# Performance work log

Measured on AMD Instinct MI355X. Metric: run time of the kernel, lower is better.

Reference implementation:

```python
import jax, jax.numpy as jnp
import numpy as np

PAD = 0
VALUE_WEIGHT = 5.0
L, D, H, DF, V, T_MAX = 8, 1024, 16, 4096, 4096, 2048
HD = D // H


def _ln(x, w, b, eps=1e-5):
    mu = x.mean(-1, keepdims=True)
    var = ((x - mu) ** 2).mean(-1, keepdims=True)
    return (x - mu) * jax.lax.rsqrt(var + eps) * w + b


def setup_inputs() -> dict:
    key = jax.random.key(0)
    ks = jax.random.split(key, 16)
    s = 0.02
    inp = {
        'input_ids': jax.random.randint(ks[0], (4, 2048), 0, V),
        'targets': jax.random.randint(ks[1], (4, 2048), 0, V),
        'value_mask': jax.random.randint(ks[2], (4, 2048), 0, 2).astype(bool),
        'token_emb': jax.random.normal(ks[3], (V, D), jnp.float32) * s,
        'pos_emb': jax.random.normal(ks[4], (T_MAX, D), jnp.float32) * s,
        'ln1_w': jnp.ones((L, D), jnp.float32), 'ln1_b': jnp.zeros((L, D), jnp.float32),
        'wqkv': jax.random.normal(ks[5], (L, D, 3 * D), jnp.float32) * s,
        'bqkv': jnp.zeros((L, 3 * D), jnp.float32),
        'wproj': jax.random.normal(ks[6], (L, D, D), jnp.float32) * s,
        'bproj': jnp.zeros((L, D), jnp.float32),
        'ln2_w': jnp.ones((L, D), jnp.float32), 'ln2_b': jnp.zeros((L, D), jnp.float32),
        'w1': jax.random.normal(ks[7], (L, D, DF), jnp.float32) * s,
        'b1': jnp.zeros((L, DF), jnp.float32),
        'w2': jax.random.normal(ks[8], (L, DF, D), jnp.float32) * s,
        'b2': jnp.zeros((L, D), jnp.float32),
        'lnf_w': jnp.ones((D,), jnp.float32), 'lnf_b': jnp.zeros((D,), jnp.float32),
    }
    return inp


def reference(input_ids, targets, value_mask, token_emb, pos_emb, ln1_w, ln1_b,
              wqkv, bqkv, wproj, bproj, ln2_w, ln2_b, w1, b1, w2, b2, lnf_w, lnf_b):
    B, T = input_ids.shape
    x = token_emb[input_ids] + pos_emb[:T]  # (B,T,D)
    causal = jnp.triu(jnp.ones((T, T), bool), 1)  # True above diagonal -> masked
    scale = 1.0 / np.sqrt(HD)
    for l in range(L):
        h = _ln(x, ln1_w[l], ln1_b[l])
        qkv = h @ wqkv[l] + bqkv[l]  # (B,T,3D)
        q, k, v = jnp.split(qkv, 3, axis=-1)
        q = q.reshape(B, T, H, HD).transpose(0, 2, 1, 3)  # (B,H,T,HD)
        k = k.reshape(B, T, H, HD).transpose(0, 2, 1, 3)
        v = v.reshape(B, T, H, HD).transpose(0, 2, 1, 3)
        scores = jnp.einsum('bhqd,bhkd->bhqk', q, k) * scale
        scores = jnp.where(causal, -jnp.inf, scores)
        attn = jax.nn.softmax(scores, axis=-1)
        out = jnp.einsum('bhqk,bhkd->bhqd', attn, v)
        out = out.transpose(0, 2, 1, 3).reshape(B, T, D)
        x = x + out @ wproj[l] + bproj[l]
        h2 = _ln(x, ln2_w[l], ln2_b[l])
        x = x + jax.nn.gelu(h2 @ w1[l] + b1[l], approximate=False) @ w2[l] + b2[l]
    x = _ln(x, lnf_w, lnf_b)
    logits = x @ token_emb.T  # tied lm_head, (B,T,V)
    # weighted CE (ignore_index=PAD zeroes the per-token loss; weights sum over all tokens)
    logp = jax.nn.log_softmax(logits, axis=-1)
    nll = -jnp.take_along_axis(logp, targets[..., None], axis=-1)[..., 0]  # (B,T)
    ce = jnp.where(targets == PAD, 0.0, nll)
    weights = 1.0 + (VALUE_WEIGHT - 1.0) * value_mask.astype(jnp.float32)
    loss = (ce * weights).sum() / weights.sum()
    return logits, loss
```

## Files before the change

kernel.cpp:

```cpp
#include <hip/hip_runtime.h>
#include <hip/hip_bf16.h>

typedef unsigned short u16;
typedef short bf16x8 __attribute__((ext_vector_type(8)));
typedef float f32x4 __attribute__((ext_vector_type(4)));

__device__ inline float bflo(unsigned int w) { union { float f; unsigned int i; } c; c.i = w << 16; return c.f; }
__device__ inline float bfhi(unsigned int w) { union { float f; unsigned int i; } c; c.i = w & 0xffff0000u; return c.f; }
__device__ inline u16 f2bf(float f) {
    union { float f; unsigned int i; } c; c.f = f;
    unsigned int r = c.i + 0x7FFFu + ((c.i >> 16) & 1u);
    return (u16)(r >> 16);
}

__device__ inline float wave_sum(float v) {
#pragma unroll
    for (int off = 32; off; off >>= 1) v += __shfl_down(v, off);
    return v;
}

__device__ inline void gload16(const void* g, void* l) {
    __builtin_amdgcn_global_load_lds((const __attribute__((address_space(1))) void*)g,
                                     (__attribute__((address_space(3))) void*)l, 16, 0, 0);
}

__global__ __launch_bounds__(256) void k_cvt(const float* __restrict__ in, u16* __restrict__ out) {
    int i = blockIdx.x * 256 + threadIdx.x;
    float4 v = ((const float4*)in)[i];
    ushort4 o;
    o.x = f2bf(v.x); o.y = f2bf(v.y); o.z = f2bf(v.z); o.w = f2bf(v.w);
    ((ushort4*)out)[i] = o;
}

__global__ __launch_bounds__(256) void k_transpose(const float* __restrict__ in, u16* __restrict__ out, int R, int C) {
    __shared__ float tile[32][33];
    const float* inL = in + (size_t)blockIdx.z * R * C;
    u16* outL = out + (size_t)blockIdx.z * R * C;
    int cb = blockIdx.x * 32, rb = blockIdx.y * 32;
    int tx = threadIdx.x, ty = threadIdx.y;
#pragma unroll
    for (int i = 0; i < 32; i += 8)
        tile[ty + i][tx] = inL[(size_t)(rb + ty + i) * C + cb + tx];
    __syncthreads();
#pragma unroll
    for (int i = 0; i < 32; i += 8)
        outL[(size_t)(cb + ty + i) * R + rb + tx] = f2bf(tile[tx][ty + i]);
}

__global__ __launch_bounds__(256) void k_embed(const int* __restrict__ ids, const float* __restrict__ emb,
                                               const float* __restrict__ pos, float* __restrict__ x) {
    int i = blockIdx.x * 256 + threadIdx.x;
    int m = i >> 8;
    int d4 = i & 255;
    int t = m & 2047;
    int id = ids[m];
    float4 e = ((const float4*)(emb + (size_t)id * 1024))[d4];
    float4 p = ((const float4*)(pos + (size_t)t * 1024))[d4];
    float4 r; r.x = e.x + p.x; r.y = e.y + p.y; r.z = e.z + p.z; r.w = e.w + p.w;
    ((float4*)(x + (size_t)m * 1024))[d4] = r;
}

__global__ __launch_bounds__(256) void k_ln(const float* __restrict__ in, const float* __restrict__ w,
                                            const float* __restrict__ b, u16* __restrict__ out) {
    int row = blockIdx.x, tid = threadIdx.x;
    float4 v = ((const float4*)(in + (size_t)row * 1024))[tid];
    float s = v.x + v.y + v.z + v.w;
    float ss = v.x * v.x + v.y * v.y + v.z * v.z + v.w * v.w;
    s = wave_sum(s); ss = wave_sum(ss);
    __shared__ float rs[4], rss[4];
    int wid = tid >> 6, lane = tid & 63;
    if (lane == 0) { rs[wid] = s; rss[wid] = ss; }
    __syncthreads();
    s = rs[0] + rs[1] + rs[2] + rs[3];
    ss = rss[0] + rss[1] + rss[2] + rss[3];
    float mu = s * (1.0f / 1024.0f);
    float var = ss * (1.0f / 1024.0f) - mu * mu;
    float inv = rsqrtf(var + 1e-5f);
    float4 wv = ((const float4*)w)[tid], bv = ((const float4*)b)[tid];
    ushort4 o;
    o.x = f2bf((v.x - mu) * inv * wv.x + bv.x);
    o.y = f2bf((v.y - mu) * inv * wv.y + bv.y);
    o.z = f2bf((v.z - mu) * inv * wv.z + bv.z);
    o.w = f2bf((v.w - mu) * inv * wv.w + bv.w);
    *(ushort4*)(out + (size_t)row * 1024 + tid * 4) = o;
}

template <bool OUT_BF16, bool GELU, bool RES, bool BIAS>
__global__ __launch_bounds__(256, 2) void k_gemm(const u16* __restrict__ A, const u16* __restrict__ Bt,
                                                 const float* __restrict__ bias, const float* __restrict__ res,
                                                 float* __restrict__ outF, u16* __restrict__ outB,
                                                 int M, int N, int K) {
    __shared__ __align__(16) u16 ldsA[128 * 32];
    __shared__ __align__(16) u16 ldsB[128 * 32];
    int tid = threadIdx.x;
    int wave = tid >> 6, lane = tid & 63;
    int quad = lane >> 4, l15 = lane & 15;
    int m0 = blockIdx.y * 128, n0 = blockIdx.x * 128;
    int wm = (wave >> 1) * 64, wn = (wave & 1) * 64;

    f32x4 acc[4][4];
#pragma unroll
    for (int i = 0; i < 4; i++)
#pragma unroll
        for (int j = 0; j < 4; j++) acc[i][j] = (f32x4){0.f, 0.f, 0.f, 0.f};

    int r0 = tid >> 2, c0 = (tid & 3) * 8;
    const size_t half = (size_t)64 * K;
    const u16* pa0 = A + (size_t)(m0 + r0) * K + c0;
    const u16* pb0 = Bt + (size_t)(n0 + r0) * K + c0;
    u16* la = ldsA + (tid & 0xC0) * 8;
    u16* lb = ldsB + (tid & 0xC0) * 8;

    for (int k0 = 0; k0 < K; k0 += 32) {
        __syncthreads();
        gload16(pa0 + k0, la);
        gload16(pa0 + half + k0, la + 2048);
        gload16(pb0 + k0, lb);
        gload16(pb0 + half + k0, lb + 2048);
        __syncthreads();
        bf16x8 af[4], bfr[4];
#pragma unroll
        for (int i = 0; i < 4; i++) af[i] = *(const bf16x8*)(ldsA + (wm + i * 16 + l15) * 32 + quad * 8);
#pragma unroll
        for (int j = 0; j < 4; j++) bfr[j] = *(const bf16x8*)(ldsB + (wn + j * 16 + l15) * 32 + quad * 8);
#pragma unroll
        for (int i = 0; i < 4; i++)
#pragma unroll
            for (int j = 0; j < 4; j++)
                acc[i][j] = __builtin_amdgcn_mfma_f32_16x16x32_bf16(af[i], bfr[j], acc[i][j], 0, 0, 0);
    }

#pragma unroll
    for (int j = 0; j < 4; j++) {
        int col = n0 + wn + j * 16 + l15;
        float bj = BIAS ? bias[col] : 0.f;
#pragma unroll
        for (int i = 0; i < 4; i++) {
#pragma unroll
            for (int r = 0; r < 4; r++) {
                int row = m0 + wm + i * 16 + quad * 4 + r;
                float v = acc[i][j][r] + bj;
                if (GELU) v = 0.5f * v * (1.0f + erff(v * 0.70710678f));
                if (RES) v += res[(size_t)row * N + col];
                if (OUT_BF16) outB[(size_t)row * N + col] = f2bf(v);
                else outF[(size_t)row * N + col] = v;
            }
        }
    }
}

__global__ __launch_bounds__(256, 4) void k_attn(const u16* __restrict__ qkv, u16* __restrict__ out) {
    const int b = blockIdx.y >> 4, h = blockIdx.y & 15;
    const int qt = gridDim.x - 1 - blockIdx.x;
    const int q0 = qt * 128;
    const int tid = threadIdx.x;
    const int wave = tid >> 6, lane = tid & 63;
    const int quad = lane >> 4, l15 = lane & 15;
    const int wrow = q0 + wave * 32;

    __shared__ __align__(16) u16 Klds[64 * 72];
    __shared__ __align__(16) u16 Vt[64 * 72];
    __shared__ __align__(16) u16 Plds[4][32 * 72];

    const u16* base = qkv + (size_t)b * 2048 * 3072 + h * 64;

    bf16x8 qf[2][2];
#pragma unroll
    for (int i = 0; i < 2; i++)
#pragma unroll
        for (int kc = 0; kc < 2; kc++)
            qf[i][kc] = *(const bf16x8*)(base + (size_t)(wrow + i * 16 + l15) * 3072 + kc * 32 + quad * 8);

    f32x4 o[2][4];
#pragma unroll
    for (int i = 0; i < 2; i++)
#pragma unroll
        for (int jd = 0; jd < 4; jd++) o[i][jd] = (f32x4){0.f, 0.f, 0.f, 0.f};
    float mrow[2][4], lrow[2][4];
#pragma unroll
    for (int i = 0; i < 2; i++)
#pragma unroll
        for (int r = 0; r < 4; r++) { mrow[i][r] = -3e38f; lrow[i][r] = 0.f; }

    const int kk_ = tid >> 2, kc0 = (tid & 3) * 16;
    const int vk = tid & 63, vc = (tid >> 6) * 16;

    const int ktiles = 2 * (qt + 1);
    for (int t = 0; t < ktiles; t++) {
        const int kt = t * 64;
        __syncthreads();
        {
            const u16* kp = base + 1024 + (size_t)(kt + kk_) * 3072 + kc0;
            uint4 a = *(const uint4*)kp;
            uint4 c = *(const uint4*)(kp + 8);
            *(uint4*)(Klds + kk_ * 72 + kc0) = a;
            *(uint4*)(Klds + kk_ * 72 + kc0 + 8) = c;
            const u16* vp = base + 2048 + (size_t)(kt + vk) * 3072 + vc;
            uint4 v0 = *(const uint4*)vp;
            uint4 v1 = *(const uint4*)(vp + 8);
            u16 tmp[16];
            *(uint4*)tmp = v0; *(uint4*)(tmp + 8) = v1;
#pragma unroll
            for (int e = 0; e < 16; e++) Vt[(vc + e) * 72 + vk] = tmp[e];
        }
        __syncthreads();

        if (kt <= wrow + 31) {
            f32x4 s[2][4];
#pragma unroll
            for (int i = 0; i < 2; i++)
#pragma unroll
                for (int j = 0; j < 4; j++) s[i][j] = (f32x4){0.f, 0.f, 0.f, 0.f};
#pragma unroll
            for (int kc = 0; kc < 2; kc++) {
                bf16x8 bf[4];
#pragma unroll
                for (int j = 0; j < 4; j++)
                    bf[j] = *(const bf16x8*)(Klds + (j * 16 + l15) * 72 + kc * 32 + quad * 8);
#pragma unroll
                for (int i = 0; i < 2; i++)
#pragma unroll
                    for (int j = 0; j < 4; j++)
                        s[i][j] = __builtin_amdgcn_mfma_f32_16x16x32_bf16(qf[i][kc], bf[j], s[i][j], 0, 0, 0);
            }
            const bool partial = (kt + 63 > wrow);
#pragma unroll
            for (int i = 0; i < 2; i++)
#pragma unroll
                for (int j = 0; j < 4; j++)
#pragma unroll
                    for (int r = 0; r < 4; r++) {
                        float v = s[i][j][r] * 0.125f;
                        if (partial) {
                            int row = wrow + i * 16 + quad * 4 + r;
                            int col = kt + j * 16 + l15;
                            if (col > row) v = -3e30f;
                        }
                        s[i][j][r] = v;
                    }
            u16* pw = Plds[wave];
#pragma unroll
            for (int i = 0; i < 2; i++)
#pragma unroll
                for (int r = 0; r < 4; r++) {
                    float mx = fmaxf(fmaxf(s[i][0][r], s[i][1][r]), fmaxf(s[i][2][r], s[i][3][r]));
                    mx = fmaxf(mx, __shfl_xor(mx, 1));
                    mx = fmaxf(mx, __shfl_xor(mx, 2));
                    mx = fmaxf(mx, __shfl_xor(mx, 4));
                    mx = fmaxf(mx, __shfl_xor(mx, 8));
                    float mnew = fmaxf(mrow[i][r], mx);
                    float alpha = __expf(mrow[i][r] - mnew);
                    mrow[i][r] = mnew;
                    float psum = 0.f;
#pragma unroll
                    for (int j = 0; j < 4; j++) {
                        float p = __expf(s[i][j][r] - mnew);
                        s[i][j][r] = p;
                        psum += p;
                    }
                    psum += __shfl_xor(psum, 1);
                    psum += __shfl_xor(psum, 2);
                    psum += __shfl_xor(psum, 4);
                    psum += __shfl_xor(psum, 8);
                    lrow[i][r] = lrow[i][r] * alpha + psum;
#pragma unroll
                    for (int jd = 0; jd < 4; jd++) o[i][jd][r] *= alpha;
                }
#pragma unroll
            for (int i = 0; i < 2; i++)
#pragma unroll
                for (int j = 0; j < 4; j++)
#pragma unroll
                    for (int r = 0; r < 4; r++)
                        pw[(i * 16 + quad * 4 + r) * 72 + j * 16 + l15] = f2bf(s[i][j][r]);
#pragma unroll
            for (int kc = 0; kc < 2; kc++) {
                bf16x8 pa[2], vb[4];
#pragma unroll
                for (int i = 0; i < 2; i++)
                    pa[i] = *(const bf16x8*)(pw + (i * 16 + l15) * 72 + kc * 32 + quad * 8);
#pragma unroll
                for (int jd = 0; jd < 4; jd++)
                    vb[jd] = *(const bf16x8*)(Vt + (jd * 16 + l15) * 72 + kc * 32 + quad * 8);
#pragma unroll
                for (int i = 0; i < 2; i++)
#pragma unroll
                    for (int jd = 0; jd < 4; jd++)
                        o[i][jd] = __builtin_amdgcn_mfma_f32_16x16x32_bf16(pa[i], vb[jd], o[i][jd], 0, 0, 0);
            }
        }
    }
#pragma unroll
    for (int i = 0; i < 2; i++)
#pragma unroll
        for (int r = 0; r < 4; r++) {
            float inv = 1.0f / lrow[i][r];
            size_t row = (size_t)(b * 2048 + wrow + i * 16 + quad * 4 + r);
#pragma unroll
            for (int jd = 0; jd < 4; jd++)
                out[row * 1024 + h * 64 + jd * 16 + l15] = f2bf(o[i][jd][r] * inv);
        }
}

__global__ __launch_bounds__(256) void k_ce(const float* __restrict__ logits, const int* __restrict__ targets,
                                            float* __restrict__ ce) {
    int row = blockIdx.x, tid = threadIdx.x;
    const float4* lr = (const float4*)(logits + (size_t)row * 4096);
    float4 v[4];
#pragma unroll
    for (int c = 0; c < 4; c++) v[c] = lr[tid + c * 256];
    float mx = -3e38f;
#pragma unroll
    for (int c = 0; c < 4; c++) mx = fmaxf(mx, fmaxf(fmaxf(v[c].x, v[c].y), fmaxf(v[c].z, v[c].w)));
#pragma unroll
    for (int off = 32; off; off >>= 1) mx = fmaxf(mx, __shfl_xor(mx, off));
    __shared__ float rm[4], rsum[4];
    int wid = tid >> 6, lane = tid & 63;
    if (lane == 0) rm[wid] = mx;
    __syncthreads();
    mx = fmaxf(fmaxf(rm[0], rm[1]), fmaxf(rm[2], rm[3]));
    float se = 0.f;
#pragma unroll
    for (int c = 0; c < 4; c++)
        se += __expf(v[c].x - mx) + __expf(v[c].y - mx) + __expf(v[c].z - mx) + __expf(v[c].w - mx);
#pragma unroll
    for (int off = 32; off; off >>= 1) se += __shfl_xor(se, off);
    if (lane == 0) rsum[wid] = se;
    __syncthreads();
    if (tid == 0) {
        se = rsum[0] + rsum[1] + rsum[2] + rsum[3];
        int tgt = targets[row];
        float nll = -(logits[(size_t)row * 4096 + tgt] - mx - logf(se));
        ce[row] = (tgt == 0) ? 0.f : nll;
    }
}

__global__ __launch_bounds__(256) void k_loss(const float* __restrict__ ce, const int* __restrict__ vmask,
                                              float* __restrict__ out) {
    int tid = threadIdx.x;
    int wid = tid >> 6, lane = tid & 63;
    int bad = 0;
    for (int i = tid; i < 2048; i += 256) {
        unsigned int w = ((const unsigned int*)vmask)[i];
        if (w > 1u) bad = 1;
    }
#pragma unroll
    for (int off = 32; off; off >>= 1) bad |= __shfl_xor(bad, off);
    __shared__ int sb[4];
    if (lane == 0) sb[wid] = bad;
    __syncthreads();
    bad = sb[0] | sb[1] | sb[2] | sb[3];

    float s1 = 0.f, s2 = 0.f;
    if (bad) {
        const unsigned char* mb = (const unsigned char*)vmask;
        for (int i = tid; i < 8192; i += 256) {
            float w = 1.0f + 4.0f * (mb[i] != 0);
            s1 += ce[i] * w; s2 += w;
        }
    } else {
        for (int i = tid; i < 8192; i += 256) {
            float w = 1.0f + 4.0f * (vmask[i] != 0);
            s1 += ce[i] * w; s2 += w;
        }
    }
#pragma unroll
    for (int off = 32; off; off >>= 1) { s1 += __shfl_down(s1, off); s2 += __shfl_down(s2, off); }
    __shared__ float r1[4], r2[4];
    if (lane == 0) { r1[wid] = s1; r2[wid] = s2; }
    __syncthreads();
    if (tid == 0) out[0] = (r1[0] + r1[1] + r1[2] + r1[3]) / (r2[0] + r2[1] + r2[2] + r2[3]);
}

extern "C" void kernel_launch(void* const* d_in, const int* in_sizes, int n_in,
                              void* d_out, int out_size, void* d_ws, size_t ws_size,
                              hipStream_t stream) {
    const int* input_ids = (const int*)d_in[0];
    const int* targets = (const int*)d_in[1];
    const int* vmask = (const int*)d_in[2];
    const float* token_emb = (const float*)d_in[3];
    const float* pos_emb = (const float*)d_in[4];
    const float* ln1_w = (const float*)d_in[5];
    const float* ln1_b = (const float*)d_in[6];
    const float* wqkv = (const float*)d_in[7];
    const float* bqkv = (const float*)d_in[8];
    const float* wproj = (const float*)d_in[9];
    const float* bproj = (const float*)d_in[10];
    const float* ln2_w = (const float*)d_in[11];
    const float* ln2_b = (const float*)d_in[12];
    const float* w1 = (const float*)d_in[13];
    const float* b1 = (const float*)d_in[14];
    const float* w2 = (const float*)d_in[15];
    const float* b2 = (const float*)d_in[16];
    const float* lnf_w = (const float*)d_in[17];
    const float* lnf_b = (const float*)d_in[18];

    char* p = (char*)d_ws;
    u16* embb = (u16*)p;   p += (size_t)4096 * 1024 * 2;
    u16* wqkvt = (u16*)p;  p += (size_t)8 * 3072 * 1024 * 2;
    u16* wprojt = (u16*)p; p += (size_t)8 * 1024 * 1024 * 2;
    u16* w1t = (u16*)p;    p += (size_t)8 * 4096 * 1024 * 2;
    u16* w2t = (u16*)p;    p += (size_t)8 * 1024 * 4096 * 2;
    float* xw = (float*)p; p += (size_t)8192 * 1024 * 4;
    u16* hb = (u16*)p;     p += (size_t)8192 * 1024 * 2;
    u16* qkvb = (u16*)p;   p += (size_t)8192 * 3072 * 2;
    u16* attnb = (u16*)p;  p += (size_t)8192 * 1024 * 2;
    u16* ffb = (u16*)p;    p += (size_t)8192 * 4096 * 2;
    float* cerow = (float*)p; p += 8192 * 4;

    float* logits = (float*)d_out;

    k_cvt<<<4096, 256, 0, stream>>>(token_emb, embb);
    dim3 tb(32, 8);
    k_transpose<<<dim3(96, 32, 8), tb, 0, stream>>>(wqkv, wqkvt, 1024, 3072);
    k_transpose<<<dim3(32, 32, 8), tb, 0, stream>>>(wproj, wprojt, 1024, 1024);
    k_transpose<<<dim3(128, 32, 8), tb, 0, stream>>>(w1, w1t, 1024, 4096);
    k_transpose<<<dim3(32, 128, 8), tb, 0, stream>>>(w2, w2t, 4096, 1024);

    k_embed<<<8192, 256, 0, stream>>>(input_ids, token_emb, pos_emb, xw);

    for (int l = 0; l < 8; l++) {
        k_ln<<<8192, 256, 0, stream>>>(xw, ln1_w + l * 1024, ln1_b + l * 1024, hb);
        k_gemm<true, false, false, true><<<dim3(24, 64), 256, 0, stream>>>(
            hb, wqkvt + (size_t)l * 3072 * 1024, bqkv + l * 3072, nullptr, nullptr, qkvb, 8192, 3072, 1024);
        k_attn<<<dim3(16, 64), 256, 0, stream>>>(qkvb, attnb);
        k_gemm<false, false, true, true><<<dim3(8, 64), 256, 0, stream>>>(
            attnb, wprojt + (size_t)l * 1024 * 1024, bproj + l * 1024, xw, xw, nullptr, 8192, 1024, 1024);
        k_ln<<<8192, 256, 0, stream>>>(xw, ln2_w + l * 1024, ln2_b + l * 1024, hb);
        k_gemm<true, true, false, true><<<dim3(32, 64), 256, 0, stream>>>(
            hb, w1t + (size_t)l * 4096 * 1024, b1 + l * 4096, nullptr, nullptr, ffb, 8192, 4096, 1024);
        k_gemm<false, false, true, true><<<dim3(8, 64), 256, 0, stream>>>(
            ffb, w2t + (size_t)l * 1024 * 4096, b2 + l * 1024, xw, xw, nullptr, 8192, 1024, 4096);
    }

    k_ln<<<8192, 256, 0, stream>>>(xw, lnf_w, lnf_b, hb);
    k_gemm<false, false, false, false><<<dim3(32, 64), 256, 0, stream>>>(
        hb, embb, nullptr, nullptr, logits, nullptr, 8192, 4096, 1024);

    k_ce<<<8192, 256, 0, stream>>>(logits, targets, cerow);
    k_loss<<<1, 256, 0, stream>>>(cerow, vmask, logits + (size_t)8192 * 4096);
}
```

Measured before the change: 5.406 ms.

## Double-buffer GEMM LDS tiles to overlap global loads with MFMA

The GEMM mainloop now uses two LDS buffers per operand. The next K-tile is issued via global_load_lds before the MFMAs on the current tile, leaving one barrier per iteration instead of two. The goal is to hide global memory latency behind compute, at the cost of doubled LDS use. The attention kernel's launch_bounds occupancy hint also drops from 4 to 2 blocks, which frees more registers per thread but may lower occupancy.

```diff
diff --git a/kernel.cpp b/kernel.cpp
--- a/kernel.cpp
+++ b/kernel.cpp
@@ -90,8 +90,8 @@
                                                  const float* __restrict__ bias, const float* __restrict__ res,
                                                  float* __restrict__ outF, u16* __restrict__ outB,
                                                  int M, int N, int K) {
-    __shared__ __align__(16) u16 ldsA[128 * 32];
-    __shared__ __align__(16) u16 ldsB[128 * 32];
+    __shared__ __align__(16) u16 ldsA[2][128 * 32];
+    __shared__ __align__(16) u16 ldsB[2][128 * 32];
     int tid = threadIdx.x;
     int wave = tid >> 6, lane = tid & 63;
     int quad = lane >> 4, l15 = lane & 15;
@@ -108,27 +108,41 @@
     const size_t half = (size_t)64 * K;
     const u16* pa0 = A + (size_t)(m0 + r0) * K + c0;
     const u16* pb0 = Bt + (size_t)(n0 + r0) * K + c0;
-    u16* la = ldsA + (tid & 0xC0) * 8;
-    u16* lb = ldsB + (tid & 0xC0) * 8;
-
-    for (int k0 = 0; k0 < K; k0 += 32) {
-        __syncthreads();
-        gload16(pa0 + k0, la);
-        gload16(pa0 + half + k0, la + 2048);
-        gload16(pb0 + k0, lb);
-        gload16(pb0 + half + k0, lb + 2048);
-        __syncthreads();
+    const int woff = (tid & 0xC0) * 8;
+
+#define STAGE(bi, k0)                              \
+    {                                              \
+        u16* la_ = ldsA[bi] + woff;                \
+        u16* lb_ = ldsB[bi] + woff;                \
+        gload16(pa0 + (k0), la_);                  \
+        gload16(pa0 + half + (k0), la_ + 2048);    \
+        gload16(pb0 + (k0), lb_);                  \
+        gload16(pb0 + half + (k0), lb_ + 2048);    \
+    }
+
+    STAGE(0, 0);
+    __syncthreads();
+
+    const int nt = K >> 5;
+    int cur = 0;
+    for (int t = 0; t < nt; t++) {
+        if (t + 1 < nt) STAGE(cur ^ 1, (t + 1) * 32);
+        const u16* ca = ldsA[cur];
+        const u16* cb = ldsB[cur];
         bf16x8 af[4], bfr[4];
 #pragma unroll
-        for (int i = 0; i < 4; i++) af[i] = *(const bf16x8*)(ldsA + (wm + i * 16 + l15) * 32 + quad * 8);
-#pragma unroll
-        for (int j = 0; j < 4; j++) bfr[j] = *(const bf16x8*)(ldsB + (wn + j * 16 + l15) * 32 + quad * 8);
+        for (int i = 0; i < 4; i++) af[i] = *(const bf16x8*)(ca + (wm + i * 16 + l15) * 32 + quad * 8);
+#pragma unroll
+        for (int j = 0; j < 4; j++) bfr[j] = *(const bf16x8*)(cb + (wn + j * 16 + l15) * 32 + quad * 8);
 #pragma unroll
         for (int i = 0; i < 4; i++)
 #pragma unroll
             for (int j = 0; j < 4; j++)
                 acc[i][j] = __builtin_amdgcn_mfma_f32_16x16x32_bf16(af[i], bfr[j], acc[i][j], 0, 0, 0);
-    }
+        __syncthreads();
+        cur ^= 1;
+    }
+#undef STAGE
 
 #pragma unroll
     for (int j = 0; j < 4; j++) {
@@ -149,7 +163,7 @@
     }
 }
 
-__global__ __launch_bounds__(256, 4) void k_attn(const u16* __restrict__ qkv, u16* __restrict__ out) {
+__global__ __launch_bounds__(256, 2) void k_attn(const u16* __restrict__ qkv, u16* __restrict__ out) {
     const int b = blockIdx.y >> 4, h = blockIdx.y & 15;
     const int qt = gridDim.x - 1 - blockIdx.x;
     const int q0 = qt * 128;
```

After: 5.170 ms. 4.4% less time.
